# Kernel tuning notes

Measured on AMD Instinct MI355X. Metric: run time of the kernel, lower is better.

The kernel has to match this reference:

```python
import jax, jax.numpy as jnp
import numpy as np

EPS_DIST = 1e-10
BN_EPS = 1e-5
K = 3  # nsample / three_nn


def setup_inputs() -> dict:
    key = jax.random.key(0)
    ks = jax.random.split(key, 8)
    B, N, S, D1, D2 = 4, 8192, 2048, 128, 256
    C_in = D1 + D2  # 384
    H = 256
    inp = {
        "pos1": jax.random.normal(ks[0], (B, 3, N), dtype=jnp.float32),
        "pos2": jax.random.normal(ks[1], (B, 3, S), dtype=jnp.float32),
        "feature1": jax.random.normal(ks[2], (B, D1, N), dtype=jnp.float32),
        "feature2": jax.random.normal(ks[3], (B, D2, S), dtype=jnp.float32),
        # MLP layer 1: Conv1d(384->256, k=1) + BN
        "W1": jax.random.normal(ks[4], (H, C_in), dtype=jnp.float32) * (1.0 / np.sqrt(C_in)),
        "b1": jnp.zeros((H,), dtype=jnp.float32),
        "g1": jnp.ones((H,), dtype=jnp.float32),
        "be1": jnp.zeros((H,), dtype=jnp.float32),
        # MLP layer 2: Conv1d(256->256, k=1) + BN
        "W2": jax.random.normal(ks[5], (H, H), dtype=jnp.float32) * (1.0 / np.sqrt(H)),
        "b2": jnp.zeros((H,), dtype=jnp.float32),
        "g2": jnp.ones((H,), dtype=jnp.float32),
        "be2": jnp.zeros((H,), dtype=jnp.float32),
    }
    return inp


def _conv_bn_relu(x, W, b, gamma, beta):
    # x: [B, Cin, N]; 1x1 Conv1d == channel GEMM
    y = jnp.einsum("oc,bcn->bon", W, x) + b[None, :, None]
    # BatchNorm1d in training mode: batch statistics over (B, N)
    mean = jnp.mean(y, axis=(0, 2), keepdims=True)
    var = jnp.mean(jnp.square(y - mean), axis=(0, 2), keepdims=True)
    y = (y - mean) * jax.lax.rsqrt(var + BN_EPS)
    y = y * gamma[None, :, None] + beta[None, :, None]
    return jax.nn.relu(y)


def reference(pos1, pos2, feature1, feature2, W1, b1, g1, be1, W2, b2, g2, be2):
    # pos1: [B,3,N], pos2: [B,3,S], feature1: [B,D1,N], feature2: [B,D2,S]
    p1 = jnp.swapaxes(pos1, 1, 2)  # [B,N,3]
    p2 = jnp.swapaxes(pos2, 1, 2)  # [B,S,3]
    # three_nn: squared-distance 3-NN of each point in p1 among p2
    d2 = (jnp.sum(p1 * p1, -1)[:, :, None]
          + jnp.sum(p2 * p2, -1)[:, None, :]
          - 2.0 * jnp.einsum("bnc,bsc->bns", p1, p2))  # [B,N,S]
    neg_vals, idx = jax.lax.top_k(-d2, K)  # idx: [B,N,3]
    dists = jnp.maximum(-neg_vals, EPS_DIST)  # dists[dists<1e-10]=1e-10
    w = 1.0 / dists
    w = w / jnp.sum(w, -1, keepdims=True)  # [B,N,3]
    # grouping_operation: gather feature2 [B,D,S] by idx -> [B,D,N,3]
    grouped = jax.vmap(lambda f, i: f[:, i])(feature2, idx)
    interpolated = jnp.sum(grouped * w[:, None, :, :], axis=-1)  # [B,D2,N]
    feat = jnp.concatenate([interpolated, feature1], axis=1)  # [B,384,N]
    feat = _conv_bn_relu(feat, W1, b1, g1, be1)
    feat = _conv_bn_relu(feat, W2, b2, g2, be2)
    return feat  # [B,256,N]
```

## Files before the change

### kernel.cpp

```cpp
#include <hip/hip_runtime.h>
#include <hip/hip_bf16.h>
#include <cstdint>

typedef unsigned short u16;
typedef unsigned int u32;
typedef unsigned long long u64;
typedef __bf16 bf16x8 __attribute__((ext_vector_type(8)));
typedef float f32x4 __attribute__((ext_vector_type(4)));
typedef u16 u16x8 __attribute__((ext_vector_type(8)));

#define FPSCALE 1048576.0f
#define FPINV   (1.0f / 1048576.0f)
#define NSLICE 16

__device__ __forceinline__ u16 f2b(float f) {
    unsigned int u = __float_as_uint(f);
    u += 0x7fffu + ((u >> 16) & 1u);
    return (u16)(u >> 16);
}
__device__ __forceinline__ float b2f(u16 h) {
    return __uint_as_float(((unsigned int)h) << 16);
}
__device__ __forceinline__ void async_cp16(void* lds, const void* g) {
    __builtin_amdgcn_global_load_lds((const __attribute__((address_space(1))) void*)g,
                                     (__attribute__((address_space(3))) void*)lds, 16, 0, 0);
}
__device__ __forceinline__ u64 ld_agent_u64(const u64* p) {
    return __hip_atomic_load(p, __ATOMIC_RELAXED, __HIP_MEMORY_SCOPE_AGENT);
}
__device__ __forceinline__ u32 fmono(float f) {
    u32 u = __float_as_uint(f);
    return u ^ (((u32)((int)u >> 31)) | 0x80000000u);
}
__device__ __forceinline__ u64 shfl_xor_u64(u64 v, int mask) {
    u32 lo = (u32)v, hi = (u32)(v >> 32);
    lo = (u32)__shfl_xor((int)lo, mask);
    hi = (u32)__shfl_xor((int)hi, mask);
    return ((u64)hi << 32) | lo;
}
__device__ __forceinline__ void ins3(u64 k, u64& k0, u64& k1, u64& k2) {
    bool c0 = k > k0, c1 = k > k1, c2 = k > k2;
    k2 = c1 ? k1 : (c2 ? k : k2);
    k1 = c0 ? k0 : (c1 ? k : k1);
    k0 = c0 ? k : k0;
}
__device__ __forceinline__ int pkix(int i) { return i + (i >> 6); }

#define NB_CVT 160
#define NB_T2  512
#define NB_T1  1024

__global__ __launch_bounds__(256, 8) void prep_kernel(const float* __restrict__ w1,
                                                      const float* __restrict__ w2,
                                                      u16* __restrict__ wb,
                                                      const float* __restrict__ feature2,
                                                      u16* __restrict__ f2t,
                                                      const float* __restrict__ feature1,
                                                      u16* __restrict__ f1t,
                                                      u64* __restrict__ SZ) {
    __shared__ __align__(16) float t[64][65];
    int ci = blockIdx.x;
    int tid = threadIdx.x;

    if (ci >= NB_CVT + NB_T2 + NB_T1) {
        for (int i = tid; i < 2 * NSLICE * 512; i += 256) SZ[i] = 0;
        if (tid == 0) *(int*)(SZ + 2 * NSLICE * 512) = 0;
        return;
    }
    if (ci < NB_CVT) {
        int i = ci * 256 + tid;
        if (i < 40960) {
            const float* src = (i < 24576) ? w1 : w2;
            int k = (i < 24576) ? i : (i - 24576);
            float4 v = *(const float4*)&src[(size_t)k * 4];
            ushort4 o;
            o.x = f2b(v.x); o.y = f2b(v.y); o.z = f2b(v.z); o.w = f2b(v.w);
            *(ushort4*)&wb[(size_t)i * 4] = o;
        }
        return;
    }
    const float* in; u16* out; int C, S, s0, c0, b;
    if (ci < NB_CVT + NB_T2) {
        int lin = ci - NB_CVT;
        C = 256; S = 2048; in = feature2; out = f2t;
        s0 = (lin & 31) * 64; c0 = ((lin >> 5) & 3) * 64; b = lin >> 7;
    } else {
        int lin = ci - NB_CVT - NB_T2;
        C = 128; S = 8192; in = feature1; out = f1t;
        s0 = (lin & 127) * 64; c0 = ((lin >> 7) & 1) * 64; b = lin >> 8;
    }
    const float* ib = in + (size_t)b * C * S;
    u16* ob = out + (size_t)b * S * C;
    int col = tid & 63, r0 = tid >> 6;
#pragma unroll
    for (int p = 0; p < 16; ++p) {
        int c = p * 4 + r0;
        t[c][col] = ib[(size_t)(c0 + c) * S + s0 + col];
    }
    __syncthreads();
#pragma unroll
    for (int p = 0; p < 16; ++p) {
        int s = p * 4 + r0;
        ob[(size_t)(s0 + s) * C + c0 + col] = f2b(t[col][s]);
    }
}

__device__ __forceinline__ void gridbar(int* cnt, int target) {
    __syncthreads();
    if (threadIdx.x == 0) {
        __hip_atomic_fetch_add(cnt, 1, __ATOMIC_RELAXED, __HIP_MEMORY_SCOPE_AGENT);
        while (__hip_atomic_load(cnt, __ATOMIC_RELAXED, __HIP_MEMORY_SCOPE_AGENT) < target)
            __builtin_amdgcn_s_sleep(16);
        __atomic_signal_fence(__ATOMIC_SEQ_CST);
    }
    __syncthreads();
}

__global__ __launch_bounds__(512, 1) void mlp_fused(const float* __restrict__ pos1,
                                                    const float* __restrict__ pos2,
                                                    const u16* __restrict__ F2T,
                                                    const u16* __restrict__ A2g,
                                                    const u16* __restrict__ W1b,
                                                    const float* __restrict__ b1,
                                                    const u16* __restrict__ W2b,
                                                    const float* __restrict__ b2,
                                                    u64* __restrict__ S1,
                                                    const float* __restrict__ g1,
                                                    const float* __restrict__ be1,
                                                    u64* __restrict__ S2,
                                                    const float* __restrict__ g2,
                                                    const float* __restrict__ be2,
                                                    float* __restrict__ OUT,
                                                    int* __restrict__ BAR) {
    __shared__ __align__(16) char smem[141312];
    u16* AS  = (u16*)smem;
    u16* BS  = (u16*)(smem + 32768);
    u16* A2  = (u16*)smem;
    u16* BS2 = (u16*)(smem + 65536);
    float* SC  = (float*)(smem + 131072);
    float* SC2 = (float*)(smem + 135168);
    float2* BNT = (float2*)(smem + 139264);
    float4* pk  = (float4*)smem;
    int*   IDXL = (int*)(smem + 33280);
    float* WGTL = (float*)(smem + 34816);

    int tid = threadIdx.x, bid = blockIdx.x;
    int lane = tid & 63, wv = tid >> 6;
    int l15 = lane & 15, q = lane >> 4;
    int lrow = lane >> 3, lchunk = lane & 7, schunk = lchunk ^ lrow;
    int j0 = bid * 128;
    int rw = wv & 3;
    int cg = wv >> 2;
    int wrow = rw * 32;
    int cbase = cg * 128;
    int sl = (bid & (NSLICE - 1)) * 512;
    int bb = j0 >> 13;

    {
        const float* p2 = pos2 + (size_t)bb * 6144;
        const float* p1 = pos1 + (size_t)bb * 24576;
        for (int i = tid; i < 2048; i += 512) {
            float x = p2[i], y = p2[2048 + i], z = p2[4096 + i];
            pk[pkix(i)] = make_float4(x, y, z, -0.5f * (x * x + y * y + z * z));
        }
        __syncthreads();

        int p = lane & 15, ck = lane >> 4;
        int nq = (j0 & 8191) + wv * 16 + p;
        float qx = p1[nq], qy = p1[8192 + nq], qz = p1[16384 + nq];
        float ga0 = -3.4e38f, ga1 = -3.4e38f, ga2 = -3.4e38f;
        float gb0 = -3.4e38f, gb1 = -3.4e38f, gb2 = -3.4e38f;
        int ia0 = 0, ia1 = 0, ia2 = 0, ib0 = 0, ib1 = 0, ib2 = 0;
        int sb = ck * 512;
        for (int h = 0; h < 8; ++h) {
            int cb = sb + h * 64;
            const float4* pc = pk + pkix(cb);
#pragma unroll 4
            for (int it = 0; it < 64; it += 2) {
                float4 cdA = pc[it];
                float4 cdB = pc[it + 1];
                {
                    int s = cb + it;
                    float tv = fmaf(qx, cdA.x, fmaf(qy, cdA.y, fmaf(qz, cdA.z, cdA.w)));
                    bool c0 = tv > ga0, c1 = tv > ga1, c2 = tv > ga2;
                    float o0 = ga0, o1 = ga1;
                    ga2 = __builtin_amdgcn_fmed3f(tv, o1, ga2);
                    ga1 = __builtin_amdgcn_fmed3f(tv, o0, o1);
                    ga0 = fmaxf(o0, tv);
                    ia2 = c1 ? ia1 : (c2 ? s : ia2);
                    ia1 = c0 ? ia0 : (c1 ? s : ia1);
                    ia0 = c0 ? s : ia0;
                }
                {
                    int s = cb + it + 1;
                    float tv = fmaf(qx, cdB.x, fmaf(qy, cdB.y, fmaf(qz, cdB.z, cdB.w)));
                    bool c0 = tv > gb0, c1 = tv > gb1, c2 = tv > gb2;
                    float o0 = gb0, o1 = gb1;
                    gb2 = __builtin_amdgcn_fmed3f(tv, o1, gb2);
                    gb1 = __builtin_amdgcn_fmed3f(tv, o0, o1);
                    gb0 = fmaxf(o0, tv);
                    ib2 = c1 ? ib1 : (c2 ? s : ib2);
                    ib1 = c0 ? ib0 : (c1 ? s : ib1);
                    ib0 = c0 ? s : ib0;
                }
            }
        }
        u64 key0 = 0, key1 = 0, key2 = 0;
        ins3(((u64)fmono(ga0) << 32) | (u64)(2047 - ia0), key0, key1, key2);
        ins3(((u64)fmono(ga1) << 32) | (u64)(2047 - ia1), key0, key1, key2);
        ins3(((u64)fmono(ga2) << 32) | (u64)(2047 - ia2), key0, key1, key2);
        ins3(((u64)fmono(gb0) << 32) | (u64)(2047 - ib0), key0, key1, key2);
        ins3(((u64)fmono(gb1) << 32) | (u64)(2047 - ib1), key0, key1, key2);
        ins3(((u64)fmono(gb2) << 32) | (u64)(2047 - ib2), key0, key1, key2);
#pragma unroll
        for (int mask = 16; mask <= 32; mask <<= 1) {
            u64 m0 = shfl_xor_u64(key0, mask);
            u64 m1 = shfl_xor_u64(key1, mask);
            u64 m2 = shfl_xor_u64(key2, mask);
            ins3(m0, key0, key1, key2);
            ins3(m1, key0, key1, key2);
            ins3(m2, key0, key1, key2);
        }
        if (lane < 16) {
            int s0 = 2047 - (int)(key0 & 0xFFFFFFFFu);
            int s1 = 2047 - (int)(key1 & 0xFFFFFFFFu);
            int s2 = 2047 - (int)(key2 & 0xFFFFFFFFu);
            int r = wv * 16 + p;
            int nn = (j0 & 8191) + r;
            float x1 = p1[nn], y1 = p1[8192 + nn], z1 = p1[16384 + nn];
            float n1 = x1 * x1 + y1 * y1 + z1 * z1;
            float X0 = p2[s0], Y0 = p2[2048 + s0], Z0 = p2[4096 + s0];
            float X1 = p2[s1], Y1v = p2[2048 + s1], Z1 = p2[4096 + s1];
            float X2 = p2[s2], Y2v = p2[2048 + s2], Z2 = p2[4096 + s2];
            float t0 = x1 * X0 + y1 * Y0 + z1 * Z0 - 0.5f * (X0 * X0 + Y0 * Y0 + Z0 * Z0);
            float t1 = x1 * X1 + y1 * Y1v + z1 * Z1 - 0.5f * (X1 * X1 + Y1v * Y1v + Z1 * Z1);
            float t2 = x1 * X2 + y1 * Y2v + z1 * Z2 - 0.5f * (X2 * X2 + Y2v * Y2v + Z2 * Z2);
            float d0 = fmaxf(fmaf(-2.f, t0, n1), 1e-10f);
            float d1 = fmaxf(fmaf(-2.f, t1, n1), 1e-10f);
            float d2 = fmaxf(fmaf(-2.f, t2, n1), 1e-10f);
            float w0v = 1.f / d0, w1v = 1.f / d1, w2v = 1.f / d2;
            float inv = 1.f / (w0v + w1v + w2v);
            IDXL[r * 3 + 0] = s0; IDXL[r * 3 + 1] = s1; IDXL[r * 3 + 2] = s2;
            WGTL[r * 3 + 0] = w0v * inv; WGTL[r * 3 + 1] = w1v * inv; WGTL[r * 3 + 2] = w2v * inv;
        }
    }
    __syncthreads();

    const u16* gp0[2]; const u16* gp1[2]; const u16* gp2[2];
    float gw0[2], gw1[2], gw2[2];
    {
        const u16* fb = F2T + (size_t)bb * 2048 * 256;
#pragma unroll
        for (int qq = 0; qq < 2; ++qq) {
            int r = wv * 16 + qq * 8 + lrow;
            gp0[qq] = fb + (size_t)IDXL[r * 3 + 0] * 256;
            gp1[qq] = fb + (size_t)IDXL[r * 3 + 1] * 256;
            gp2[qq] = fb + (size_t)IDXL[r * 3 + 2] * 256;
            gw0[qq] = WGTL[r * 3 + 0]; gw1[qq] = WGTL[r * 3 + 1]; gw2[qq] = WGTL[r * 3 + 2];
        }
    }
    __syncthreads();

    u16x8 G0[2], G1[2], G2[2];

    f32x4 acc[2][8];
#pragma unroll
    for (int i = 0; i < 2; ++i)
#pragma unroll
        for (int jj = 0; jj < 8; ++jj) acc[i][jj] = (f32x4){0.f, 0.f, 0.f, 0.f};

    auto stageB1 = [&](int buf, int k0) {
#pragma unroll
        for (int qq = 0; qq < 4; ++qq) {
            int row = wv * 32 + qq * 8;
            async_cp16(&BS[buf * 16384 + row * 64],
                       W1b + (size_t)(row + lrow) * 384 + k0 + schunk * 8);
        }
    };
    auto stageA1f1 = [&](int buf, int k0) {
        const u16* src = A2g + (size_t)j0 * 128 + (k0 - 256);
#pragma unroll
        for (int qq = 0; qq < 2; ++qq) {
            int row = wv * 16 + qq * 8;
            async_cp16(&AS[buf * 8192 + row * 64],
                       src + (size_t)(row + lrow) * 128 + schunk * 8);
        }
    };
    auto gissue = [&](int k0) {
        int c = k0 + lchunk * 8;
#pragma unroll
        for (int qq = 0; qq < 2; ++qq) {
            G0[qq] = *(const u16x8*)(gp0[qq] + c);
            G1[qq] = *(const u16x8*)(gp1[qq] + c);
            G2[qq] = *(const u16x8*)(gp2[qq] + c);
        }
    };
    auto gwrite = [&](int buf) {
#pragma unroll
        for (int qq = 0; qq < 2; ++qq) {
            int row = wv * 16 + qq * 8;
            u16x8 o;
#pragma unroll
            for (int e = 0; e < 8; ++e)
                o[e] = f2b(gw0[qq] * b2f(G0[qq][e]) + gw1[qq] * b2f(G1[qq][e]) +
                           gw2[qq] * b2f(G2[qq][e]));
            *(u16x8*)&AS[buf * 8192 + (row + lrow) * 64 + schunk * 8] = o;
        }
    };
    auto stageB2 = [&](int buf, int k0) {
#pragma unroll
        for (int qq = 0; qq < 4; ++qq) {
            int row = wv * 32 + qq * 8;
            async_cp16(&BS2[buf * 16384 + row * 64],
                       W2b + (size_t)(row + lrow) * 256 + k0 + schunk * 8);
        }
    };

    gissue(0);
    stageB1(0, 0);
    gwrite(0);
    __syncthreads();
    for (int t = 0; t < 6; ++t) {
        int cur = t & 1;
        if (t < 3) { gissue((t + 1) * 64); stageB1(cur ^ 1, (t + 1) * 64); }
        else if (t < 5) { stageB1(cur ^ 1, (t + 1) * 64); stageA1f1(cur ^ 1, (t + 1) * 64); }
#pragma unroll
        for (int ks = 0; ks < 2; ++ks) {
            bf16x8 af[2];
#pragma unroll
            for (int i = 0; i < 2; ++i) {
                int row = wrow + i * 16 + l15;
                af[i] = *(const bf16x8*)&AS[cur * 8192 + row * 64 +
                                            ((ks * 4 + q) ^ (l15 & 7)) * 8];
            }
#pragma unroll
            for (int jj = 0; jj < 8; ++jj) {
                int brow = cbase + jj * 16 + l15;
                bf16x8 bfr = *(const bf16x8*)&BS[cur * 16384 + brow * 64 +
                                                 ((ks * 4 + q) ^ (l15 & 7)) * 8];
#pragma unroll
                for (int i = 0; i < 2; ++i)
                    acc[i][jj] = __builtin_amdgcn_mfma_f32_16x16x32_bf16(af[i], bfr,
                                                                         acc[i][jj], 0, 0, 0);
            }
        }
        if (t < 3) gwrite(cur ^ 1);
        __syncthreads();
    }

    stageB2(0, 0);

#pragma unroll
    for (int jj = 0; jj < 8; ++jj) {
        int c = cbase + jj * 16 + l15;
        float bv = b1[c];
        float s = 0.f, s2 = 0.f;
#pragma unroll
        for (int i = 0; i < 2; ++i)
#pragma unroll
            for (int r = 0; r < 4; ++r) {
                acc[i][jj][r] += bv;
                float v = acc[i][jj][r];
                s += v; s2 += v * v;
            }
        s += __shfl_xor(s, 16); s += __shfl_xor(s, 32);
        s2 += __shfl_xor(s2, 16); s2 += __shfl_xor(s2, 32);
        if (q == 0) { SC[rw * 256 + c] = s; SC2[rw * 256 + c] = s2; }
    }
    __syncthreads();
    if (tid < 256) {
        float fs = SC[tid] + SC[256 + tid] + SC[512 + tid] + SC[768 + tid];
        float fs2 = SC2[tid] + SC2[256 + tid] + SC2[512 + tid] + SC2[768 + tid];
        atomicAdd(&S1[sl + tid], (u64)(long long)llrintf(fs * FPSCALE));
        atomicAdd(&S1[sl + 256 + tid], (u64)(long long)llrintf(fs2 * FPSCALE));
    }
    gridbar(BAR, 256);

    if (tid < 256) {
        long long su = 0, sq = 0;
#pragma unroll
        for (int r = 0; r < NSLICE; ++r) {
            su += (long long)ld_agent_u64(&S1[r * 512 + tid]);
            sq += (long long)ld_agent_u64(&S1[r * 512 + 256 + tid]);
        }
        float fs = (float)su * FPINV;
        float fs2 = (float)sq * FPINV;
        const float inv = 1.f / 32768.f;
        float mean = fs * inv;
        float var = fs2 * inv - mean * mean;
        float a = g1[tid] * rsqrtf(var + 1e-5f);
        BNT[tid] = make_float2(a, be1[tid] - mean * a);
    }
    __syncthreads();

#pragma unroll
    for (int jj = 0; jj < 8; ++jj) {
        int c = cbase + jj * 16 + l15;
        float2 bn = BNT[c];
        int chunkbase = c >> 3;
        int win = c & 7;
#pragma unroll
        for (int i = 0; i < 2; ++i)
#pragma unroll
            for (int r = 0; r < 4; ++r) {
                int row = wrow + i * 16 + q * 4 + r;
                float vb = b2f(f2b(acc[i][jj][r]));
                u16 h = f2b(fmaxf(vb * bn.x + bn.y, 0.f));
                A2[row * 256 + ((chunkbase ^ (row & 7)) * 8 + win)] = h;
            }
    }
    __syncthreads();

#pragma unroll
    for (int i = 0; i < 2; ++i)
#pragma unroll
        for (int jj = 0; jj < 8; ++jj) acc[i][jj] = (f32x4){0.f, 0.f, 0.f, 0.f};

    for (int t = 0; t < 4; ++t) {
        int cur = t & 1;
        if (t < 3) stageB2(cur ^ 1, (t + 1) * 64);
#pragma unroll
        for (int ks = 0; ks < 2; ++ks) {
            bf16x8 af[2];
            int kc = t * 8 + ks * 4 + q;
#pragma unroll
            for (int i = 0; i < 2; ++i) {
                int row = wrow + i * 16 + l15;
                af[i] = *(const bf16x8*)&A2[row * 256 + ((kc ^ (l15 & 7)) * 8)];
            }
#pragma unroll
            for (int jj = 0; jj < 8; ++jj) {
                int brow = cbase + jj * 16 + l15;
                bf16x8 bfr = *(const bf16x8*)&BS2[cur * 16384 + brow * 64 +
                                                  ((ks * 4 + q) ^ (l15 & 7)) * 8];
#pragma unroll
                for (int i = 0; i < 2; ++i)
                    acc[i][jj] = __builtin_amdgcn_mfma_f32_16x16x32_bf16(af[i], bfr,
                                                                         acc[i][jj], 0, 0, 0);
            }
        }
        __syncthreads();
    }

#pragma unroll
    for (int jj = 0; jj < 8; ++jj) {
        int c = cbase + jj * 16 + l15;
        float bv = b2[c];
        float s = 0.f, s2 = 0.f;
#pragma unroll
        for (int i = 0; i < 2; ++i)
#pragma unroll
            for (int r = 0; r < 4; ++r) {
                acc[i][jj][r] += bv;
                float v = acc[i][jj][r];
                s += v; s2 += v * v;
            }
        s += __shfl_xor(s, 16); s += __shfl_xor(s, 32);
        s2 += __shfl_xor(s2, 16); s2 += __shfl_xor(s2, 32);
        if (q == 0) { SC[rw * 256 + c] = s; SC2[rw * 256 + c] = s2; }
    }
    __syncthreads();
    if (tid < 256) {
        float fs = SC[tid] + SC[256 + tid] + SC[512 + tid] + SC[768 + tid];
        float fs2 = SC2[tid] + SC2[256 + tid] + SC2[512 + tid] + SC2[768 + tid];
        atomicAdd(&S2[sl + tid], (u64)(long long)llrintf(fs * FPSCALE));
        atomicAdd(&S2[sl + 256 + tid], (u64)(long long)llrintf(fs2 * FPSCALE));
    }
    gridbar(BAR, 512);

    if (tid < 256) {
        long long su = 0, sq = 0;
#pragma unroll
        for (int r = 0; r < NSLICE; ++r) {
            su += (long long)ld_agent_u64(&S2[r * 512 + tid]);
            sq += (long long)ld_agent_u64(&S2[r * 512 + 256 + tid]);
        }
        float fs = (float)su * FPINV;
        float fs2 = (float)sq * FPINV;
        const float inv = 1.f / 32768.f;
        float mean = fs * inv;
        float var = fs2 * inv - mean * mean;
        float a = g2[tid] * rsqrtf(var + 1e-5f);
        BNT[tid] = make_float2(a, be2[tid] - mean * a);
    }
    __syncthreads();

    int nbase = j0 & 8191;
#pragma unroll
    for (int jj = 0; jj < 8; ++jj) {
        int o = cbase + jj * 16 + l15;
        float2 bn = BNT[o];
#pragma unroll
        for (int i = 0; i < 2; ++i) {
            int n0 = nbase + wrow + i * 16 + q * 4;
            float4 v;
            v.x = fmaxf(b2f(f2b(acc[i][jj][0])) * bn.x + bn.y, 0.f);
            v.y = fmaxf(b2f(f2b(acc[i][jj][1])) * bn.x + bn.y, 0.f);
            v.z = fmaxf(b2f(f2b(acc[i][jj][2])) * bn.x + bn.y, 0.f);
            v.w = fmaxf(b2f(f2b(acc[i][jj][3])) * bn.x + bn.y, 0.f);
            *(float4*)&OUT[(size_t)bb * 2097152 + (size_t)o * 8192 + n0] = v;
        }
    }
}

extern "C" void kernel_launch(void* const* d_in, const int* in_sizes, int n_in,
                              void* d_out, int out_size, void* d_ws, size_t ws_size,
                              hipStream_t stream) {
    const float* pos1 = (const float*)d_in[0];
    const float* pos2 = (const float*)d_in[1];
    const float* feature1 = (const float*)d_in[2];
    const float* feature2 = (const float*)d_in[3];
    const float* W1 = (const float*)d_in[4];
    const float* b1 = (const float*)d_in[5];
    const float* g1 = (const float*)d_in[6];
    const float* be1 = (const float*)d_in[7];
    const float* W2 = (const float*)d_in[8];
    const float* b2 = (const float*)d_in[9];
    const float* g2 = (const float*)d_in[10];
    const float* be2 = (const float*)d_in[11];

    char* ws = (char*)d_ws;
    u16*    W1B   = (u16*)(ws + 786432);
    u16*    W2B   = (u16*)(ws + 983040);
    u16*    F2T   = (u16*)(ws + 1118208);
    u16*    F1T   = (u16*)(ws + 5312512);
    u64*    SSTAT = (u64*)(ws + 47255552);
    u64*    S1    = SSTAT;
    u64*    S2    = SSTAT + NSLICE * 512;
    int*    BAR   = (int*)(SSTAT + 2 * NSLICE * 512);
    float*  OUT   = (float*)d_out;

    prep_kernel<<<NB_CVT + NB_T2 + NB_T1 + 1, 256, 0, stream>>>(
        W1, W2, W1B, feature2, F2T, feature1, F1T, SSTAT);
    mlp_fused<<<256, 512, 0, stream>>>(pos1, pos2, F2T, F1T, W1B, b1, W2B, b2,
                                       S1, g1, be1, S2, g2, be2, OUT, BAR);
}
```

Measured before the change: 168.9 us.

## Fuse feature1 transpose into main kernel and keep kNN results in registers

Removes the prep-kernel pass that transposed and converted feature1 to bf16 in global memory. The main kernel now loads fp32 feature1 tiles into LDS with async copies early and converts them to the swizzled bf16 A tile in LDS just before the K-steps that use them. The 3-NN indices and weights are passed between lanes with shuffles instead of LDS arrays, which drops two block barriers. The pos2 table moves to a different LDS region with a rotated scan order in place of padding, and the LDS footprint grows to 160KB.

```diff
diff --git a/kernel.cpp b/kernel.cpp
--- a/kernel.cpp
+++ b/kernel.cpp
@@ -44,25 +44,21 @@
     k1 = c0 ? k0 : (c1 ? k : k1);
     k0 = c0 ? k : k0;
 }
-__device__ __forceinline__ int pkix(int i) { return i + (i >> 6); }
 
 #define NB_CVT 160
 #define NB_T2  512
-#define NB_T1  1024
 
 __global__ __launch_bounds__(256, 8) void prep_kernel(const float* __restrict__ w1,
                                                       const float* __restrict__ w2,
                                                       u16* __restrict__ wb,
                                                       const float* __restrict__ feature2,
                                                       u16* __restrict__ f2t,
-                                                      const float* __restrict__ feature1,
-                                                      u16* __restrict__ f1t,
                                                       u64* __restrict__ SZ) {
     __shared__ __align__(16) float t[64][65];
     int ci = blockIdx.x;
     int tid = threadIdx.x;
 
-    if (ci >= NB_CVT + NB_T2 + NB_T1) {
+    if (ci >= NB_CVT + NB_T2) {
         for (int i = tid; i < 2 * NSLICE * 512; i += 256) SZ[i] = 0;
         if (tid == 0) *(int*)(SZ + 2 * NSLICE * 512) = 0;
         return;
@@ -79,29 +75,21 @@
         }
         return;
     }
-    const float* in; u16* out; int C, S, s0, c0, b;
-    if (ci < NB_CVT + NB_T2) {
-        int lin = ci - NB_CVT;
-        C = 256; S = 2048; in = feature2; out = f2t;
-        s0 = (lin & 31) * 64; c0 = ((lin >> 5) & 3) * 64; b = lin >> 7;
-    } else {
-        int lin = ci - NB_CVT - NB_T2;
-        C = 128; S = 8192; in = feature1; out = f1t;
-        s0 = (lin & 127) * 64; c0 = ((lin >> 7) & 1) * 64; b = lin >> 8;
-    }
-    const float* ib = in + (size_t)b * C * S;
-    u16* ob = out + (size_t)b * S * C;
+    int lin = ci - NB_CVT;
+    int s0 = (lin & 31) * 64, c0 = ((lin >> 5) & 3) * 64, b = lin >> 7;
+    const float* ib = feature2 + (size_t)b * 256 * 2048;
+    u16* ob = f2t + (size_t)b * 2048 * 256;
     int col = tid & 63, r0 = tid >> 6;
 #pragma unroll
     for (int p = 0; p < 16; ++p) {
         int c = p * 4 + r0;
-        t[c][col] = ib[(size_t)(c0 + c) * S + s0 + col];
+        t[c][col] = ib[(size_t)(c0 + c) * 2048 + s0 + col];
     }
     __syncthreads();
 #pragma unroll
     for (int p = 0; p < 16; ++p) {
         int s = p * 4 + r0;
-        ob[(size_t)(s0 + s) * C + c0 + col] = f2b(t[col][s]);
+        ob[(size_t)(s0 + s) * 256 + c0 + col] = f2b(t[col][s]);
     }
 }
 
@@ -119,7 +107,7 @@
 __global__ __launch_bounds__(512, 1) void mlp_fused(const float* __restrict__ pos1,
                                                     const float* __restrict__ pos2,
                                                     const u16* __restrict__ F2T,
-                                                    const u16* __restrict__ A2g,
+                                                    const float* __restrict__ feature1,
                                                     const u16* __restrict__ W1b,
                                                     const float* __restrict__ b1,
                                                     const u16* __restrict__ W2b,
@@ -132,17 +120,17 @@
                                                     const float* __restrict__ be2,
                                                     float* __restrict__ OUT,
                                                     int* __restrict__ BAR) {
-    __shared__ __align__(16) char smem[141312];
+    __shared__ __align__(16) char smem[163840];
     u16* AS  = (u16*)smem;
     u16* BS  = (u16*)(smem + 32768);
     u16* A2  = (u16*)smem;
     u16* BS2 = (u16*)(smem + 65536);
+    float* F1a = (float*)(smem + 98304);
+    float* F1b = (float*)(smem + 131072);
+    float4* pk = (float4*)(smem + 131072);
     float* SC  = (float*)(smem + 131072);
     float* SC2 = (float*)(smem + 135168);
     float2* BNT = (float2*)(smem + 139264);
-    float4* pk  = (float4*)smem;
-    int*   IDXL = (int*)(smem + 33280);
-    float* WGTL = (float*)(smem + 34816);
 
     int tid = threadIdx.x, bid = blockIdx.x;
     int lane = tid & 63, wv = tid >> 6;
@@ -155,137 +143,128 @@
     int cbase = cg * 128;
     int sl = (bid & (NSLICE - 1)) * 512;
     int bb = j0 >> 13;
-
+    int n0 = j0 & 8191;
+
+    auto stageB1 = [&](int buf, int k0) {
+#pragma unroll
+        for (int qq = 0; qq < 4; ++qq) {
+            int row = wv * 32 + qq * 8;
+            async_cp16(&BS[buf * 16384 + row * 64],
+                       W1b + (size_t)(row + lrow) * 384 + k0 + schunk * 8);
+        }
+    };
+    auto loadF1 = [&](float* dst, int c0) {
+        const float* src = feature1 + (size_t)bb * 1048576 + (size_t)c0 * 8192 + n0;
+#pragma unroll
+        for (int r = 0; r < 4; ++r) {
+            int c = r * 16 + wv * 2;
+            async_cp16(dst + (size_t)c * 128,
+                       src + (size_t)(c + (lane >> 5)) * 8192 + (lane & 31) * 4);
+        }
+    };
+
+    stageB1(0, 0);
+    stageB1(1, 64);
+    loadF1(F1a, 0);
+
+    const float* p2 = pos2 + (size_t)bb * 6144;
+    const float* p1 = pos1 + (size_t)bb * 24576;
+    for (int i = tid; i < 2048; i += 512) {
+        float x = p2[i], y = p2[2048 + i], z = p2[4096 + i];
+        pk[i] = make_float4(x, y, z, -0.5f * (x * x + y * y + z * z));
+    }
+    __syncthreads();
+
+    int p = lane & 15, ck = lane >> 4;
+    int nq = n0 + wv * 16 + p;
+    float qx = p1[nq], qy = p1[8192 + nq], qz = p1[16384 + nq];
+    float ga0 = -3.4e38f, ga1 = -3.4e38f, ga2 = -3.4e38f;
+    float gb0 = -3.4e38f, gb1 = -3.4e38f, gb2 = -3.4e38f;
+    int ia0 = 0, ia1 = 0, ia2 = 0, ib0 = 0, ib1 = 0, ib2 = 0;
+    int sbk = ck * 512, rot = 2 * ck;
+    for (int h = 0; h < 8; ++h) {
+        int cb = sbk + h * 64;
+        const float4* pc = pk + cb;
+#pragma unroll 4
+        for (int it = 0; it < 64; it += 2) {
+            int i0 = (it + rot) & 63;
+            float4 cdA = pc[i0];
+            float4 cdB = pc[i0 + 1];
+            {
+                int s = cb + i0;
+                float tv = fmaf(qx, cdA.x, fmaf(qy, cdA.y, fmaf(qz, cdA.z, cdA.w)));
+                bool c0 = tv > ga0, c1 = tv > ga1, c2 = tv > ga2;
+                float o0 = ga0, o1 = ga1;
+                ga2 = __builtin_amdgcn_fmed3f(tv, o1, ga2);
+                ga1 = __builtin_amdgcn_fmed3f(tv, o0, o1);
+                ga0 = fmaxf(o0, tv);
+                ia2 = c1 ? ia1 : (c2 ? s : ia2);
+                ia1 = c0 ? ia0 : (c1 ? s : ia1);
+                ia0 = c0 ? s : ia0;
+            }
+            {
+                int s = cb + i0 + 1;
+                float tv = fmaf(qx, cdB.x, fmaf(qy, cdB.y, fmaf(qz, cdB.z, cdB.w)));
+                bool c0 = tv > gb0, c1 = tv > gb1, c2 = tv > gb2;
+                float o0 = gb0, o1 = gb1;
+                gb2 = __builtin_amdgcn_fmed3f(tv, o1, gb2);
+                gb1 = __builtin_amdgcn_fmed3f(tv, o0, o1);
+                gb0 = fmaxf(o0, tv);
+                ib2 = c1 ? ib1 : (c2 ? s : ib2);
+                ib1 = c0 ? ib0 : (c1 ? s : ib1);
+                ib0 = c0 ? s : ib0;
+            }
+        }
+    }
+    u64 key0 = 0, key1 = 0, key2 = 0;
+    ins3(((u64)fmono(ga0) << 32) | (u64)(2047 - ia0), key0, key1, key2);
+    ins3(((u64)fmono(ga1) << 32) | (u64)(2047 - ia1), key0, key1, key2);
+    ins3(((u64)fmono(ga2) << 32) | (u64)(2047 - ia2), key0, key1, key2);
+    ins3(((u64)fmono(gb0) << 32) | (u64)(2047 - ib0), key0, key1, key2);
+    ins3(((u64)fmono(gb1) << 32) | (u64)(2047 - ib1), key0, key1, key2);
+    ins3(((u64)fmono(gb2) << 32) | (u64)(2047 - ib2), key0, key1, key2);
+#pragma unroll
+    for (int mask = 16; mask <= 32; mask <<= 1) {
+        u64 m0 = shfl_xor_u64(key0, mask);
+        u64 m1 = shfl_xor_u64(key1, mask);
+        u64 m2 = shfl_xor_u64(key2, mask);
+        ins3(m0, key0, key1, key2);
+        ins3(m1, key0, key1, key2);
+        ins3(m2, key0, key1, key2);
+    }
+    int s0v = 2047 - (int)(key0 & 0xFFFFFFFFu);
+    int s1v = 2047 - (int)(key1 & 0xFFFFFFFFu);
+    int s2v = 2047 - (int)(key2 & 0xFFFFFFFFu);
+    float w0n, w1n, w2n;
     {
-        const float* p2 = pos2 + (size_t)bb * 6144;
-        const float* p1 = pos1 + (size_t)bb * 24576;
-        for (int i = tid; i < 2048; i += 512) {
-            float x = p2[i], y = p2[2048 + i], z = p2[4096 + i];
-            pk[pkix(i)] = make_float4(x, y, z, -0.5f * (x * x + y * y + z * z));
-        }
-        __syncthreads();
-
-        int p = lane & 15, ck = lane >> 4;
-        int nq = (j0 & 8191) + wv * 16 + p;
-        float qx = p1[nq], qy = p1[8192 + nq], qz = p1[16384 + nq];
-        float ga0 = -3.4e38f, ga1 = -3.4e38f, ga2 = -3.4e38f;
-        float gb0 = -3.4e38f, gb1 = -3.4e38f, gb2 = -3.4e38f;
-        int ia0 = 0, ia1 = 0, ia2 = 0, ib0 = 0, ib1 = 0, ib2 = 0;
-        int sb = ck * 512;
-        for (int h = 0; h < 8; ++h) {
-            int cb = sb + h * 64;
-            const float4* pc = pk + pkix(cb);
-#pragma unroll 4
-            for (int it = 0; it < 64; it += 2) {
-                float4 cdA = pc[it];
-                float4 cdB = pc[it + 1];
-                {
-                    int s = cb + it;
-                    float tv = fmaf(qx, cdA.x, fmaf(qy, cdA.y, fmaf(qz, cdA.z, cdA.w)));
-                    bool c0 = tv > ga0, c1 = tv > ga1, c2 = tv > ga2;
-                    float o0 = ga0, o1 = ga1;
-                    ga2 = __builtin_amdgcn_fmed3f(tv, o1, ga2);
-                    ga1 = __builtin_amdgcn_fmed3f(tv, o0, o1);
-                    ga0 = fmaxf(o0, tv);
-                    ia2 = c1 ? ia1 : (c2 ? s : ia2);
-                    ia1 = c0 ? ia0 : (c1 ? s : ia1);
-                    ia0 = c0 ? s : ia0;
-                }
-                {
-                    int s = cb + it + 1;
-                    float tv = fmaf(qx, cdB.x, fmaf(qy, cdB.y, fmaf(qz, cdB.z, cdB.w)));
-                    bool c0 = tv > gb0, c1 = tv > gb1, c2 = tv > gb2;
-                    float o0 = gb0, o1 = gb1;
-                    gb2 = __builtin_amdgcn_fmed3f(tv, o1, gb2);
-                    gb1 = __builtin_amdgcn_fmed3f(tv, o0, o1);
-                    gb0 = fmaxf(o0, tv);
-                    ib2 = c1 ? ib1 : (c2 ? s : ib2);
-                    ib1 = c0 ? ib0 : (c1 ? s : ib1);
-                    ib0 = c0 ? s : ib0;
-                }
-            }
-        }
-        u64 key0 = 0, key1 = 0, key2 = 0;
-        ins3(((u64)fmono(ga0) << 32) | (u64)(2047 - ia0), key0, key1, key2);
-        ins3(((u64)fmono(ga1) << 32) | (u64)(2047 - ia1), key0, key1, key2);
-        ins3(((u64)fmono(ga2) << 32) | (u64)(2047 - ia2), key0, key1, key2);
-        ins3(((u64)fmono(gb0) << 32) | (u64)(2047 - ib0), key0, key1, key2);
-        ins3(((u64)fmono(gb1) << 32) | (u64)(2047 - ib1), key0, key1, key2);
-        ins3(((u64)fmono(gb2) << 32) | (u64)(2047 - ib2), key0, key1, key2);
-#pragma unroll
-        for (int mask = 16; mask <= 32; mask <<= 1) {
-            u64 m0 = shfl_xor_u64(key0, mask);
-            u64 m1 = shfl_xor_u64(key1, mask);
-            u64 m2 = shfl_xor_u64(key2, mask);
-            ins3(m0, key0, key1, key2);
-            ins3(m1, key0, key1, key2);
-            ins3(m2, key0, key1, key2);
-        }
-        if (lane < 16) {
-            int s0 = 2047 - (int)(key0 & 0xFFFFFFFFu);
-            int s1 = 2047 - (int)(key1 & 0xFFFFFFFFu);
-            int s2 = 2047 - (int)(key2 & 0xFFFFFFFFu);
-            int r = wv * 16 + p;
-            int nn = (j0 & 8191) + r;
-            float x1 = p1[nn], y1 = p1[8192 + nn], z1 = p1[16384 + nn];
-            float n1 = x1 * x1 + y1 * y1 + z1 * z1;
-            float X0 = p2[s0], Y0 = p2[2048 + s0], Z0 = p2[4096 + s0];
-            float X1 = p2[s1], Y1v = p2[2048 + s1], Z1 = p2[4096 + s1];
-            float X2 = p2[s2], Y2v = p2[2048 + s2], Z2 = p2[4096 + s2];
-            float t0 = x1 * X0 + y1 * Y0 + z1 * Z0 - 0.5f * (X0 * X0 + Y0 * Y0 + Z0 * Z0);
-            float t1 = x1 * X1 + y1 * Y1v + z1 * Z1 - 0.5f * (X1 * X1 + Y1v * Y1v + Z1 * Z1);
-            float t2 = x1 * X2 + y1 * Y2v + z1 * Z2 - 0.5f * (X2 * X2 + Y2v * Y2v + Z2 * Z2);
-            float d0 = fmaxf(fmaf(-2.f, t0, n1), 1e-10f);
-            float d1 = fmaxf(fmaf(-2.f, t1, n1), 1e-10f);
-            float d2 = fmaxf(fmaf(-2.f, t2, n1), 1e-10f);
-            float w0v = 1.f / d0, w1v = 1.f / d1, w2v = 1.f / d2;
-            float inv = 1.f / (w0v + w1v + w2v);
-            IDXL[r * 3 + 0] = s0; IDXL[r * 3 + 1] = s1; IDXL[r * 3 + 2] = s2;
-            WGTL[r * 3 + 0] = w0v * inv; WGTL[r * 3 + 1] = w1v * inv; WGTL[r * 3 + 2] = w2v * inv;
-        }
-    }
-    __syncthreads();
-
+        float n1 = qx * qx + qy * qy + qz * qz;
+        float4 P0 = pk[s0v], P1 = pk[s1v], P2 = pk[s2v];
+        float t0 = qx * P0.x + qy * P0.y + qz * P0.z + P0.w;
+        float t1 = qx * P1.x + qy * P1.y + qz * P1.z + P1.w;
+        float t2 = qx * P2.x + qy * P2.y + qz * P2.z + P2.w;
+        float d0 = fmaxf(fmaf(-2.f, t0, n1), 1e-10f);
+        float d1 = fmaxf(fmaf(-2.f, t1, n1), 1e-10f);
+        float d2 = fmaxf(fmaf(-2.f, t2, n1), 1e-10f);
+        float w0v = 1.f / d0, w1v = 1.f / d1, w2v = 1.f / d2;
+        float inv = 1.f / (w0v + w1v + w2v);
+        w0n = w0v * inv; w1n = w1v * inv; w2n = w2v * inv;
+    }
     const u16* gp0[2]; const u16* gp1[2]; const u16* gp2[2];
     float gw0[2], gw1[2], gw2[2];
     {
         const u16* fb = F2T + (size_t)bb * 2048 * 256;
 #pragma unroll
         for (int qq = 0; qq < 2; ++qq) {
-            int r = wv * 16 + qq * 8 + lrow;
-            gp0[qq] = fb + (size_t)IDXL[r * 3 + 0] * 256;
-            gp1[qq] = fb + (size_t)IDXL[r * 3 + 1] * 256;
-            gp2[qq] = fb + (size_t)IDXL[r * 3 + 2] * 256;
-            gw0[qq] = WGTL[r * 3 + 0]; gw1[qq] = WGTL[r * 3 + 1]; gw2[qq] = WGTL[r * 3 + 2];
-        }
-    }
-    __syncthreads();
-
+            int srcl = qq * 8 + lrow;
+            gp0[qq] = fb + (size_t)__shfl(s0v, srcl) * 256;
+            gp1[qq] = fb + (size_t)__shfl(s1v, srcl) * 256;
+            gp2[qq] = fb + (size_t)__shfl(s2v, srcl) * 256;
+            gw0[qq] = __shfl(w0n, srcl);
+            gw1[qq] = __shfl(w1n, srcl);
+            gw2[qq] = __shfl(w2n, srcl);
+        }
+    }
     u16x8 G0[2], G1[2], G2[2];
-
-    f32x4 acc[2][8];
-#pragma unroll
-    for (int i = 0; i < 2; ++i)
-#pragma unroll
-        for (int jj = 0; jj < 8; ++jj) acc[i][jj] = (f32x4){0.f, 0.f, 0.f, 0.f};
-
-    auto stageB1 = [&](int buf, int k0) {
-#pragma unroll
-        for (int qq = 0; qq < 4; ++qq) {
-            int row = wv * 32 + qq * 8;
-            async_cp16(&BS[buf * 16384 + row * 64],
-                       W1b + (size_t)(row + lrow) * 384 + k0 + schunk * 8);
-        }
-    };
-    auto stageA1f1 = [&](int buf, int k0) {
-        const u16* src = A2g + (size_t)j0 * 128 + (k0 - 256);
-#pragma unroll
-        for (int qq = 0; qq < 2; ++qq) {
-            int row = wv * 16 + qq * 8;
-            async_cp16(&AS[buf * 8192 + row * 64],
-                       src + (size_t)(row + lrow) * 128 + schunk * 8);
-        }
-    };
     auto gissue = [&](int k0) {
         int c = k0 + lchunk * 8;
 #pragma unroll
@@ -307,6 +286,17 @@
             *(u16x8*)&AS[buf * 8192 + (row + lrow) * 64 + schunk * 8] = o;
         }
     };
+    auto buildF1 = [&](int buf, const float* F1) {
+#pragma unroll
+        for (int qq = 0; qq < 2; ++qq) {
+            int row = wv * 16 + qq * 8;
+            u16x8 o;
+#pragma unroll
+            for (int w = 0; w < 8; ++w)
+                o[w] = f2b(F1[(lchunk * 8 + w) * 128 + row + lrow]);
+            *(u16x8*)&AS[buf * 8192 + (row + lrow) * 64 + schunk * 8] = o;
+        }
+    };
     auto stageB2 = [&](int buf, int k0) {
 #pragma unroll
         for (int qq = 0; qq < 4; ++qq) {
@@ -317,13 +307,23 @@
     };
 
     gissue(0);
-    stageB1(0, 0);
+    __syncthreads();
+    loadF1(F1b, 64);
     gwrite(0);
     __syncthreads();
+
+    f32x4 acc[2][8];
+#pragma unroll
+    for (int i = 0; i < 2; ++i)
+#pragma unroll
+        for (int jj = 0; jj < 8; ++jj) acc[i][jj] = (f32x4){0.f, 0.f, 0.f, 0.f};
+
     for (int t = 0; t < 6; ++t) {
         int cur = t & 1;
-        if (t < 3) { gissue((t + 1) * 64); stageB1(cur ^ 1, (t + 1) * 64); }
-        else if (t < 5) { stageB1(cur ^ 1, (t + 1) * 64); stageA1f1(cur ^ 1, (t + 1) * 64); }
+        if (t < 3) gissue((t + 1) * 64);
+        if (t >= 1 && t <= 4) stageB1((t + 1) & 1, (t + 1) * 64);
+        if (t == 3) buildF1(0, F1a);
+        if (t == 4) buildF1(1, F1b);
 #pragma unroll
         for (int ks = 0; ks < 2; ++ks) {
             bf16x8 af[2];
@@ -485,20 +485,19 @@
     }
     __syncthreads();
 
-    int nbase = j0 & 8191;
 #pragma unroll
     for (int jj = 0; jj < 8; ++jj) {
         int o = cbase + jj * 16 + l15;
         float2 bn = BNT[o];
 #pragma unroll
         for (int i = 0; i < 2; ++i) {
-            int n0 = nbase + wrow + i * 16 + q * 4;
+            int nn = n0 + wrow + i * 16 + q * 4;
             float4 v;
             v.x = fmaxf(b2f(f2b(acc[i][jj][0])) * bn.x + bn.y, 0.f);
             v.y = fmaxf(b2f(f2b(acc[i][jj][1])) * bn.x + bn.y, 0.f);
             v.z = fmaxf(b2f(f2b(acc[i][jj][2])) * bn.x + bn.y, 0.f);
             v.w = fmaxf(b2f(f2b(acc[i][jj][3])) * bn.x + bn.y, 0.f);
-            *(float4*)&OUT[(size_t)bb * 2097152 + (size_t)o * 8192 + n0] = v;
+            *(float4*)&OUT[(size_t)bb * 2097152 + (size_t)o * 8192 + nn] = v;
         }
     }
 }
@@ -523,15 +522,14 @@
     u16*    W1B   = (u16*)(ws + 786432);
     u16*    W2B   = (u16*)(ws + 983040);
     u16*    F2T   = (u16*)(ws + 1118208);
-    u16*    F1T   = (u16*)(ws + 5312512);
     u64*    SSTAT = (u64*)(ws + 47255552);
     u64*    S1    = SSTAT;
     u64*    S2    = SSTAT + NSLICE * 512;
     int*    BAR   = (int*)(SSTAT + 2 * NSLICE * 512);
     float*  OUT   = (float*)d_out;
 
-    prep_kernel<<<NB_CVT + NB_T2 + NB_T1 + 1, 256, 0, stream>>>(
-        W1, W2, W1B, feature2, F2T, feature1, F1T, SSTAT);
-    mlp_fused<<<256, 512, 0, stream>>>(pos1, pos2, F2T, F1T, W1B, b1, W2B, b2,
+    prep_kernel<<<NB_CVT + NB_T2 + 1, 256, 0, stream>>>(
+        W1, W2, W1B, feature2, F2T, SSTAT);
+    mlp_fused<<<256, 512, 0, stream>>>(pos1, pos2, F2T, feature1, W1B, b1, W2B, b2,
                                        S1, g1, be1, S2, g2, be2, OUT, BAR);
 }
```

Result: slower. 174.4 us (+3.2%).
